# Kernel tuning notes

Measured on AMD Instinct MI355X. Metric: run time of the kernel, lower is better.

## Reference

```python
import jax, jax.numpy as jnp
import numpy as np

# dims
H = 2048      # hidden_size
NH = 16       # num q heads
NKV = 8       # num kv heads
D = 128       # head_dim
E = 16        # routed experts
K = 4         # top_k
I = 1024      # moe_intermediate_size (per routed expert)
SI = 1024     # shared expert intermediate (moe_intermediate * num_shared)
T = 2048      # tokens
EPS = 1e-5
THETA = 10000.0
RSF = 1.0     # router_scaling_factor


def setup_inputs() -> dict:
    key = jax.random.key(0)
    ks = jax.random.split(key, 10)
    s = 0.02
    return {
        "positions": jnp.arange(T, dtype=jnp.int32),
        "hidden_states": jax.random.normal(ks[0], (T, H), jnp.float32),
        "qkv_w": jax.random.normal(ks[1], (H, (NH + 2 * NKV) * D), jnp.float32) * s,
        "o_w": jax.random.normal(ks[2], (NH * D, H), jnp.float32) * s,
        "q_norm_w": jnp.ones((D,), jnp.float32),
        "k_norm_w": jnp.ones((D,), jnp.float32),
        "ln1_w": jnp.ones((H,), jnp.float32),
        "ln2_w": jnp.ones((H,), jnp.float32),
        "gate_w": jax.random.normal(ks[3], (H, E), jnp.float32) * s,
        "expert_bias": jax.random.normal(ks[4], (E,), jnp.float32) * 0.1,
        "shared_gu_w": jax.random.normal(ks[5], (H, 2 * SI), jnp.float32) * s,
        "shared_down_w": jax.random.normal(ks[6], (SI, H), jnp.float32) * s,
        "exp_gu_w": jax.random.normal(ks[7], (E, H, 2 * I), jnp.float32) * s,
        "exp_down_w": jax.random.normal(ks[8], (E, I, H), jnp.float32) * s,
    }


def _rmsnorm(x, w):
    v = jnp.mean(x * x, axis=-1, keepdims=True)
    return x * jax.lax.rsqrt(v + EPS) * w


def _rope(x, cos, sin):
    # neox style: rotate halves. x: [T, heads, D]; cos/sin: [T, 1, D//2]
    x1, x2 = x[..., : D // 2], x[..., D // 2 :]
    return jnp.concatenate([x1 * cos - x2 * sin, x2 * cos + x1 * sin], axis=-1)


def reference(positions, hidden_states, qkv_w, o_w, q_norm_w, k_norm_w,
              ln1_w, ln2_w, gate_w, expert_bias, shared_gu_w, shared_down_w,
              exp_gu_w, exp_down_w):
    hs = hidden_states
    # --- attention block ---
    x = _rmsnorm(hs, ln1_w)
    qkv = x @ qkv_w
    q = qkv[:, : NH * D].reshape(T, NH, D)
    k = qkv[:, NH * D : NH * D + NKV * D].reshape(T, NKV, D)
    v = qkv[:, NH * D + NKV * D :].reshape(T, NKV, D)
    # per-head qk RMSNorm
    q = _rmsnorm(q, q_norm_w)
    k = _rmsnorm(k, k_norm_w)
    # rotary embedding
    inv_freq = 1.0 / (THETA ** (jnp.arange(0, D, 2, dtype=jnp.float32) / D))
    ang = positions.astype(jnp.float32)[:, None] * inv_freq  # [T, D/2]
    cos = jnp.cos(ang)[:, None, :]
    sin = jnp.sin(ang)[:, None, :]
    q = _rope(q, cos, sin)
    k = _rope(k, cos, sin)
    # GQA: repeat kv heads
    rep = NH // NKV
    k = jnp.repeat(k, rep, axis=1)  # [T, NH, D]
    v = jnp.repeat(v, rep, axis=1)
    scores = jnp.einsum('qhd,khd->hqk', q, k) * (D ** -0.5)
    causal = jnp.tril(jnp.ones((T, T), dtype=bool))
    scores = jnp.where(causal[None], scores, -1e30)
    attn = jax.nn.softmax(scores, axis=-1)
    ao = jnp.einsum('hqk,khd->qhd', attn, v).reshape(T, NH * D)
    h = hs + ao @ o_w
    # --- MoE block ---
    x2 = _rmsnorm(h, ln2_w)
    router_logits = x2 @ gate_w  # fp32 gate
    sig = jax.nn.sigmoid(router_logits)
    biased = sig + expert_bias  # correction bias only used for selection
    _, top_idx = jax.lax.top_k(biased, K)  # [T, K]
    w = jnp.take_along_axis(sig, top_idx, axis=-1)
    w = w / jnp.sum(w, axis=-1, keepdims=True) * RSF  # renormalize + routed scaling
    combine = jnp.sum(jax.nn.one_hot(top_idx, E, dtype=x2.dtype) * w[..., None], axis=1)  # [T, E]
    # routed experts (dense-masked reference for the grouped GEMM)
    gu = jnp.einsum('th,ehi->eti', x2, exp_gu_w)  # [E, T, 2I]
    act = jax.nn.silu(gu[..., :I]) * gu[..., I:]
    routed = jnp.einsum('eti,eih->eth', act, exp_down_w)
    routed = jnp.einsum('eth,te->th', routed, combine)
    # shared expert
    sgu = x2 @ shared_gu_w
    shared = (jax.nn.silu(sgu[:, :SI]) * sgu[:, SI:]) @ shared_down_w
    return h + routed + shared
```

## Files before the change

kernel.cpp:

```cpp
#include <hip/hip_runtime.h>
#include <math.h>

#define T_ 2048
#define H_ 2048
#define NH_ 16
#define NKV_ 8
#define D_ 128
#define E_ 16
#define I_ 1024
#define SI_ 1024

typedef _Float16 half8 __attribute__((ext_vector_type(8)));
typedef _Float16 half4_t __attribute__((ext_vector_type(4)));
typedef float f32x4 __attribute__((ext_vector_type(4)));

#define MFMA32(a,b,c) __builtin_amdgcn_mfma_f32_16x16x32_f16((a),(b),(c),0,0,0)

__device__ __constant__ float LO_S = 2048.0f;
__device__ __constant__ float LO_I = 1.0f/2048.0f;
#define EPS_ 1e-5f

#define GL16(gp, lp) __builtin_amdgcn_global_load_lds( \
    (const __attribute__((address_space(1))) unsigned int*)(const void*)(gp), \
    (__attribute__((address_space(3))) unsigned int*)(void*)(lp), 16, 0, 0)

__global__ void tables_k(const int* __restrict__ pos, float* __restrict__ cosT, float* __restrict__ sinT) {
  int t = blockIdx.x;
  int j = threadIdx.x;
  float pf = (float)pow(10000.0, (double)j / 64.0);
  float invf = 1.0f / pf;
  float ang = (float)pos[t] * invf;
  cosT[t*64 + j] = (float)cos((double)ang);
  sinT[t*64 + j] = (float)sin((double)ang);
}

__global__ __launch_bounds__(256) void rmsnorm_k(const float* __restrict__ x, const float* __restrict__ w,
                                                 _Float16* __restrict__ oh, _Float16* __restrict__ ol) {
  int row = blockIdx.x;
  const float* xr = x + (size_t)row * H_;
  int tid = threadIdx.x;
  float4 a = *(const float4*)(xr + tid*8);
  float4 b = *(const float4*)(xr + tid*8 + 4);
  float ss = a.x*a.x + a.y*a.y + a.z*a.z + a.w*a.w + b.x*b.x + b.y*b.y + b.z*b.z + b.w*b.w;
  #pragma unroll
  for (int m = 1; m < 64; m <<= 1) ss += __shfl_xor(ss, m);
  __shared__ float wsum[4];
  int wid = tid >> 6, lane = tid & 63;
  if (lane == 0) wsum[wid] = ss;
  __syncthreads();
  float tot = wsum[0] + wsum[1] + wsum[2] + wsum[3];
  float rinv = 1.0f / sqrtf(tot / (float)H_ + EPS_);
  const float* av = (const float*)&a;
  const float* bv = (const float*)&b;
  #pragma unroll
  for (int j = 0; j < 8; ++j) {
    float xv = (j < 4) ? av[j] : bv[j-4];
    float val = xv * rinv * w[tid*8 + j];
    _Float16 h = (_Float16)val;
    size_t o = (size_t)row*H_ + tid*8 + j;
    oh[o] = h;
    ol[o] = (_Float16)((val - (float)h) * LO_S);
  }
}

__global__ __launch_bounds__(128) void qkvpost_k(
    const float* __restrict__ qkv, const float* __restrict__ qnw, const float* __restrict__ knw,
    const float* __restrict__ cosT, const float* __restrict__ sinT,
    _Float16* __restrict__ qh, _Float16* __restrict__ ql,
    _Float16* __restrict__ kh, _Float16* __restrict__ kl,
    _Float16* __restrict__ vth, _Float16* __restrict__ vtl) {
  int t = blockIdx.x, u = blockIdx.y, d = threadIdx.x;
  float val = qkv[(size_t)t*4096 + u*128 + d];
  __shared__ float sv[128];
  __shared__ float ssum[2];
  if (u < 24) {
    float ss = val * val;
    #pragma unroll
    for (int m = 1; m < 64; m <<= 1) ss += __shfl_xor(ss, m);
    if ((d & 63) == 0) ssum[d >> 6] = ss;
    __syncthreads();
    float rinv = 1.0f / sqrtf((ssum[0] + ssum[1]) / 128.0f + EPS_);
    const float* nw = (u < 16) ? qnw : knw;
    float nv = val * rinv * nw[d];
    sv[d] = nv;
    __syncthreads();
    int j = d & 63;
    float c = cosT[t*64 + j], s = sinT[t*64 + j];
    float x1 = sv[j], x2 = sv[j + 64];
    float o = (d < 64) ? (x1*c - x2*s) : (x2*c + x1*s);
    _Float16 hv = (_Float16)o;
    _Float16 lv = (_Float16)((o - (float)hv) * LO_S);
    if (u < 16) { size_t off = ((size_t)u*T_ + t)*D_ + d; qh[off] = hv; ql[off] = lv; }
    else { size_t off = ((size_t)(u-16)*T_ + t)*D_ + d; kh[off] = hv; kl[off] = lv; }
  } else {
    int kv = u - 24;
    _Float16 hv = (_Float16)val;
    _Float16 lv = (_Float16)((val - (float)hv) * LO_S);
    size_t off = ((size_t)kv*D_ + d)*T_ + t;
    vth[off] = hv; vtl[off] = lv;
  }
}

template<bool SPL>
__global__ __launch_bounds__(256) void transpose_k(const float* __restrict__ in, _Float16* __restrict__ oh,
                                                   _Float16* __restrict__ ol, int R, int C) {
  size_t zo = (size_t)blockIdx.z * R * C;
  in += zo; oh += zo; if (SPL) ol += zo;
  __shared__ float tile[64][68];
  const int c0 = blockIdx.x*64, r0 = blockIdx.y*64;
  const int tid = threadIdx.x;
  const int lr = tid >> 4;
  const int lc = (tid & 15) * 4;
  #pragma unroll
  for (int rg = 0; rg < 4; ++rg) {
    float4 v = *(const float4*)(in + (size_t)(r0 + rg*16 + lr)*C + c0 + lc);
    *(float4*)&tile[rg*16 + lr][lc] = v;
  }
  __syncthreads();
  const int orow = tid >> 2;
  const int oc   = (tid & 3) * 16;
  half8 h0v, h1v, l0v, l1v;
  #pragma unroll
  for (int j = 0; j < 16; ++j) {
    float f = tile[oc + j][orow];
    _Float16 h = (_Float16)f;
    if (j < 8) { h0v[j] = h; if (SPL) l0v[j] = (_Float16)((f - (float)h) * LO_S); }
    else       { h1v[j-8] = h; if (SPL) l1v[j-8] = (_Float16)((f - (float)h) * LO_S); }
  }
  const size_t ob = (size_t)(c0 + orow)*R + r0 + oc;
  *(half8*)(oh + ob)     = h0v;
  *(half8*)(oh + ob + 8) = h1v;
  if (SPL) { *(half8*)(ol + ob) = l0v; *(half8*)(ol + ob + 8) = l1v; }
}

__global__ __launch_bounds__(256) void transpose_gu_k(const float* __restrict__ in, _Float16* __restrict__ out,
                                                      int R, int Ih) {
  size_t zi = (size_t)blockIdx.z * R * 2 * Ih;
  in += zi; out += zi;
  __shared__ float tg[64][36], tu[64][36];
  const int j0 = blockIdx.x*32, h0 = blockIdx.y*64;
  const int tid = threadIdx.x;
  const int lh = tid >> 2;
  const int lj = (tid & 3) * 8;
  const int C = 2*Ih;
  const float* src = in + (size_t)(h0 + lh)*C + j0 + lj;
  float4 ga = *(const float4*)(src);
  float4 gb = *(const float4*)(src + 4);
  float4 ua = *(const float4*)(src + Ih);
  float4 ub = *(const float4*)(src + Ih + 4);
  *(float4*)&tg[lh][lj]   = ga;
  *(float4*)&tg[lh][lj+4] = gb;
  *(float4*)&tu[lh][lj]   = ua;
  *(float4*)&tu[lh][lj+4] = ub;
  __syncthreads();
  const int oj = tid >> 3;
  const int p  = (tid >> 2) & 1;
  const int oc = (tid & 3) * 16;
  float (*sel)[36] = p ? tu : tg;
  half8 a, b;
  #pragma unroll
  for (int j = 0; j < 16; ++j) {
    float f = sel[oc + j][oj];
    if (j < 8) a[j] = (_Float16)f; else b[j-8] = (_Float16)f;
  }
  const size_t ob = (size_t)(2*(j0 + oj) + p)*R + h0 + oc;
  *(half8*)(out + ob)     = a;
  *(half8*)(out + ob + 8) = b;
}

__global__ __launch_bounds__(256) void attn_k(
    const _Float16* __restrict__ qh_, const _Float16* __restrict__ ql_,
    const _Float16* __restrict__ kh_, const _Float16* __restrict__ kl_,
    const _Float16* __restrict__ vh_, const _Float16* __restrict__ vl_,
    _Float16* __restrict__ aoh, _Float16* __restrict__ aol) {
  __shared__ _Float16 sK [2][4096];
  __shared__ _Float16 sKl[2][4096];
  __shared__ _Float16 sV [2][4096];
  __shared__ _Float16 sVl[2][4096];
  const int head = blockIdx.x;
  const int y = blockIdx.y;
  const int tile = (y < 16) ? (31 - 2*y) : (2*(y-16));
  const int kvh = head >> 1;
  const int wid = threadIdx.x >> 6, lane = threadIdx.x & 63;
  const int fr = lane & 15, fs = lane >> 4;
  const float scale = 0.08838834764831845f;

  const char* kbC  = (const char*)(kh_ + (size_t)kvh*T_*D_);
  const char* kbCl = (const char*)(kl_ + (size_t)kvh*T_*D_);
  const char* vbC  = (const char*)(vh_ + (size_t)kvh*D_*T_);
  const char* vbCl = (const char*)(vl_ + (size_t)kvh*D_*T_);

  auto stage = [&](int buf, int kvt) {
    #pragma unroll
    for (int i = 0; i < 2; ++i) {
      const int off  = wid*2048 + i*1024;
      const int loff = off + lane*16;
      const int r  = loff >> 8;
      const int u  = (loff >> 4) & 15;
      const int us = u ^ (r & 7);
      const size_t gb = ((size_t)(kvt + r) << 8) + ((size_t)us << 4);
      GL16(kbC  + gb, (char*)&sK [buf][0] + off);
      GL16(kbCl + gb, (char*)&sKl[buf][0] + off);
      const int d   = loff >> 6;
      const int uv  = (loff >> 4) & 3;
      const int uvs = uv ^ ((d >> 2) & 3);
      const size_t gvb = (size_t)d*(T_*2) + (size_t)kvt*2 + ((size_t)uvs << 4);
      GL16(vbC  + gvb, (char*)&sV [buf][0] + off);
      GL16(vbCl + gvb, (char*)&sVl[buf][0] + off);
    }
  };

  const int q0 = tile*64 + wid*16;
  const int qrow = q0 + fr;
  const _Float16* qb_  = qh_ + ((size_t)head*T_ + qrow)*D_;
  const _Float16* qlb_ = ql_ + ((size_t)head*T_ + qrow)*D_;
  half8 qf[4], qfl[4];
  #pragma unroll
  for (int s = 0; s < 4; ++s) {
    qf[s]  = *(const half8*)(qb_  + s*32 + fs*8);
    qfl[s] = *(const half8*)(qlb_ + s*32 + fs*8);
  }
  float m = -1e30f, lsum = 0.f;
  f32x4 oacc[8] = {};
  f32x4 oacc2[8] = {};
  const int nc = 2*tile + 2;

  stage(0, 0);
  #pragma unroll 1
  for (int c = 0; c < nc; ++c) {
    const int kvt = c*32;
    const int buf = c & 1;
    __syncthreads();
    if (c + 1 < nc) stage(buf ^ 1, kvt + 32);

    f32x4 sa = {0,0,0,0}, sa2 = {0,0,0,0}, sb = {0,0,0,0}, sb2 = {0,0,0,0};
    __builtin_amdgcn_s_setprio(1);
    #pragma unroll
    for (int s = 0; s < 4; ++s) {
      const int rA = fr, rB = fr + 16;
      const int eA = (((4*s + fs) ^ (rA & 7)) << 3);
      const int eB = (((4*s + fs) ^ (rB & 7)) << 3);
      half8 kfA  = *(const half8*)&sK [buf][rA*128 + eA];
      half8 kflA = *(const half8*)&sKl[buf][rA*128 + eA];
      half8 kfB  = *(const half8*)&sK [buf][rB*128 + eB];
      half8 kflB = *(const half8*)&sKl[buf][rB*128 + eB];
      sa  = MFMA32(kfA, qf[s], sa);
      sa2 = MFMA32(kfA, qfl[s], sa2);
      sa2 = MFMA32(kflA, qf[s], sa2);
      sb  = MFMA32(kfB, qf[s], sb);
      sb2 = MFMA32(kfB, qfl[s], sb2);
      sb2 = MFMA32(kflB, qf[s], sb2);
    }
    __builtin_amdgcn_s_setprio(0);

    float sv[8];
    #pragma unroll
    for (int r = 0; r < 4; ++r) {
      float xA = (sa[r] + sa2[r]*LO_I) * scale;
      sv[r] = (kvt + fs*4 + r > qrow) ? -INFINITY : xA;
      float xB = (sb[r] + sb2[r]*LO_I) * scale;
      sv[4+r] = (kvt + 16 + fs*4 + r > qrow) ? -INFINITY : xB;
    }
    float tm = -INFINITY;
    #pragma unroll
    for (int j = 0; j < 8; ++j) tm = fmaxf(tm, sv[j]);
    tm = fmaxf(tm, __shfl_xor(tm, 16));
    tm = fmaxf(tm, __shfl_xor(tm, 32));
    if (tm > m + 8.f) {
      float f = __expf(m - tm);
      lsum *= f;
      #pragma unroll
      for (int db = 0; db < 8; ++db) { oacc[db] *= f; oacc2[db] *= f; }
      m = tm;
    }
    float p[8]; float ps = 0.f;
    #pragma unroll
    for (int j = 0; j < 8; ++j) { p[j] = __expf(sv[j] - m); ps += p[j]; }
    ps += __shfl_xor(ps, 16);
    ps += __shfl_xor(ps, 32);
    lsum += ps;
    half8 ph, pl;
    #pragma unroll
    for (int j = 0; j < 8; ++j) {
      _Float16 hp = (_Float16)p[j];
      ph[j] = hp;
      pl[j] = (_Float16)((p[j] - (float)hp) * LO_S);
    }

    __builtin_amdgcn_s_setprio(1);
    #pragma unroll
    for (int db = 0; db < 8; ++db) {
      const int d0 = db*16 + fr;
      const int base = d0*32;
      const int sw = (d0 >> 2) & 3;
      const int e1 = ((((fs>>1)    ) ^ sw) << 3) + (fs & 1)*4;
      const int e2 = (((2 + (fs>>1)) ^ sw) << 3) + (fs & 1)*4;
      half4_t v0  = *(const half4_t*)&sV [buf][base + e1];
      half4_t v1  = *(const half4_t*)&sV [buf][base + e2];
      half4_t v0l = *(const half4_t*)&sVl[buf][base + e1];
      half4_t v1l = *(const half4_t*)&sVl[buf][base + e2];
      half8 vf, vfl;
      #pragma unroll
      for (int j = 0; j < 4; ++j) { vf[j] = v0[j]; vf[4+j] = v1[j]; vfl[j] = v0l[j]; vfl[4+j] = v1l[j]; }
      oacc[db]  = MFMA32(vf, ph, oacc[db]);
      oacc2[db] = MFMA32(vf, pl, oacc2[db]);
      oacc2[db] = MFMA32(vfl, ph, oacc2[db]);
    }
    __builtin_amdgcn_s_setprio(0);
  }

  float inv = 1.0f / lsum;
  #pragma unroll
  for (int db = 0; db < 8; ++db) {
    #pragma unroll
    for (int r = 0; r < 4; ++r) {
      float val = (oacc[db][r] + oacc2[db][r]*LO_I) * inv;
      int dd = db*16 + fs*4 + r;
      size_t off = (size_t)qrow*(NH_*D_) + head*D_ + dd;
      _Float16 hv = (_Float16)val;
      aoh[off] = hv;
      aol[off] = (_Float16)((val - (float)hv) * LO_S);
    }
  }
}

__global__ __launch_bounds__(256) void router_k(const _Float16* __restrict__ x2h, const _Float16* __restrict__ x2l,
    const float* __restrict__ gw, const float* __restrict__ eb,
    int* __restrict__ cnt, int* __restrict__ list, float* __restrict__ wl) {
  int t = blockIdx.x*4 + (threadIdx.x >> 6);
  int lane = threadIdx.x & 63;
  const _Float16* xh = x2h + (size_t)t*H_;
  const _Float16* xl = x2l + (size_t)t*H_;
  f32x4 a0 = {0,0,0,0}, a1 = {0,0,0,0}, a2 = {0,0,0,0}, a3 = {0,0,0,0};
  for (int h = lane; h < H_; h += 64) {
    float xv = (float)xh[h] + (float)xl[h] * LO_I;
    const float* g = gw + (size_t)h*16;
    a0 += xv * (*(const f32x4*)(g));
    a1 += xv * (*(const f32x4*)(g+4));
    a2 += xv * (*(const f32x4*)(g+8));
    a3 += xv * (*(const f32x4*)(g+12));
  }
  float acc[16];
  #pragma unroll
  for (int j = 0; j < 4; ++j) { acc[j]=a0[j]; acc[4+j]=a1[j]; acc[8+j]=a2[j]; acc[12+j]=a3[j]; }
  #pragma unroll
  for (int mm = 1; mm < 64; mm <<= 1) {
    #pragma unroll
    for (int e2 = 0; e2 < 16; ++e2) acc[e2] += __shfl_xor(acc[e2], mm);
  }
  if (lane == 0) {
    float sig[16], biased[16];
    #pragma unroll
    for (int e2 = 0; e2 < 16; ++e2) {
      float s = 1.0f / (1.0f + expf(-acc[e2]));
      sig[e2] = s; biased[e2] = s + eb[e2];
    }
    int sel[4]; float wv[4]; float wsum = 0.f;
    unsigned used = 0;
    for (int j = 0; j < 4; ++j) {
      int bi = -1; float bv = -1e30f;
      for (int e2 = 0; e2 < 16; ++e2)
        if (!((used >> e2) & 1) && biased[e2] > bv) { bv = biased[e2]; bi = e2; }
      used |= 1u << bi;
      sel[j] = bi; wv[j] = sig[bi]; wsum += sig[bi];
    }
    for (int j = 0; j < 4; ++j) {
      int e2 = sel[j];
      int pos = atomicAdd(&cnt[e2], 1);
      list[e2*T_ + pos] = t;
      wl[e2*T_ + pos] = wv[j] / wsum;
    }
  }
}

__global__ void scan_k(const int* __restrict__ cnt, int* __restrict__ base) {
  if (threadIdx.x == 0 && blockIdx.x == 0) {
    int s = 0;
    for (int e2 = 0; e2 < 16; ++e2) { base[e2] = s; s += cnt[e2]; }
  }
}

struct GArgs {
  const _Float16* Ah; const _Float16* Al;
  const _Float16* Bh; const _Float16* Bl;
  int M, N, K;
  const int* rowlist; const float* wlist; const int* cnt; const int* base;
  float* C; const float* res; _Float16* act; float* outAt; int ldc;
};

template<int MODE, bool SPLIT, int DEPTH>
__global__ __launch_bounds__(512, 4) void gemm_k(GArgs p) {
  constexpr int LPS = SPLIT ? 4 : 2;
  const int e = blockIdx.z;
  const int M = p.cnt ? p.cnt[e] : p.M;
  const int m0 = blockIdx.y * 128;
  if (m0 >= M) return;
  const int n0 = blockIdx.x * 128;
  const int tid = threadIdx.x;
  const int wid = tid >> 6, lane = tid & 63;

  __shared__ _Float16 sA[DEPTH][4096];
  __shared__ _Float16 sB[DEPTH][4096];
  __shared__ _Float16 sAl[SPLIT ? DEPTH : 1][SPLIT ? 4096 : 8];
  __shared__ _Float16 sBl[SPLIT ? DEPTH : 1][SPLIT ? 4096 : 8];

  const int srow = tid >> 2;
  const int slot = ((tid & 3) ^ (srow & 3)) * 16;
  const int ldsOff = wid * 1024;
  size_t aIdx;
  if constexpr (MODE == 2) {
    if (p.rowlist) {
      int tok = p.rowlist[(size_t)e * T_ + m0 + srow];
      tok = tok < 0 ? 0 : (tok > T_ - 1 ? T_ - 1 : tok);
      aIdx = (size_t)tok;
    } else aIdx = (size_t)(m0 + srow);
  } else if constexpr (MODE == 3) {
    aIdx = (size_t)p.base[e] + m0 + srow;
  } else {
    aIdx = (size_t)(m0 + srow);
  }
  const char* aPtr  = (const char*)(p.Ah + aIdx * (size_t)p.K) + slot;
  const char* alPtr = SPLIT ? (const char*)(p.Al + aIdx * (size_t)p.K) + slot : aPtr;
  const size_t bIdx = (size_t)e * p.N + n0 + srow;
  const char* bPtr  = (const char*)(p.Bh + bIdx * (size_t)p.K) + slot;
  const char* blPtr = SPLIT ? (const char*)(p.Bl + bIdx * (size_t)p.K) + slot : bPtr;

  auto stage = [&](int buf, int kb) {
    GL16(aPtr + kb, (char*)&sA[buf][0] + ldsOff);
    GL16(bPtr + kb, (char*)&sB[buf][0] + ldsOff);
    if constexpr (SPLIT) {
      GL16(alPtr + kb, (char*)&sAl[buf][0] + ldsOff);
      GL16(blPtr + kb, (char*)&sBl[buf][0] + ldsOff);
    }
  };

  const int wr = (wid >> 2) * 64, wc = (wid & 3) * 32;
  const int fr = lane & 15, fs = lane >> 4;

  f32x4 acc[4][2] = {};
  f32x4 acc2[4][2] = {};

  const int nt = p.K >> 5;
  stage(0, 0);
  if constexpr (DEPTH == 3) { if (nt > 1) stage(1, 64); }

  for (int t = 0; t < nt; ++t) {
    if constexpr (DEPTH == 3) {
      if (t + 2 < nt) stage((t + 2) % 3, (t + 2) * 64);
      __builtin_amdgcn_sched_barrier(0);
      if (t + 2 < nt)      asm volatile("s_waitcnt vmcnt(%0)" :: "i"(2*LPS) : "memory");
      else if (t + 1 < nt) asm volatile("s_waitcnt vmcnt(%0)" :: "i"(LPS)   : "memory");
      else                 asm volatile("s_waitcnt vmcnt(0)" ::: "memory");
    } else {
      if (t + 1 < nt) {
        stage((t + 1) & 1, (t + 1) * 64);
        __builtin_amdgcn_sched_barrier(0);
        asm volatile("s_waitcnt vmcnt(%0)" :: "i"(LPS) : "memory");
      } else {
        __builtin_amdgcn_sched_barrier(0);
        asm volatile("s_waitcnt vmcnt(0)" ::: "memory");
      }
    }
    __builtin_amdgcn_s_barrier();
    __builtin_amdgcn_sched_barrier(0);

    const int cb = (DEPTH == 3) ? (t % 3) : (t & 1);
    half8 ah[4], bh[2], al[4], bl[2];
    #pragma unroll
    for (int i = 0; i < 4; ++i) {
      const int pa = (fs ^ ((wr + i*16 + fr) & 3)) * 8;
      ah[i] = *(const half8*)&sA[cb][(wr + i*16 + fr)*32 + pa];
      if constexpr (SPLIT) al[i] = *(const half8*)&sAl[cb][(wr + i*16 + fr)*32 + pa];
    }
    #pragma unroll
    for (int i = 0; i < 2; ++i) {
      const int pb = (fs ^ ((wc + i*16 + fr) & 3)) * 8;
      bh[i] = *(const half8*)&sB[cb][(wc + i*16 + fr)*32 + pb];
      if constexpr (SPLIT) bl[i] = *(const half8*)&sBl[cb][(wc + i*16 + fr)*32 + pb];
    }
    __builtin_amdgcn_s_setprio(1);
    #pragma unroll
    for (int mi = 0; mi < 4; ++mi) {
      #pragma unroll
      for (int ni = 0; ni < 2; ++ni) {
        acc[mi][ni] = MFMA32(ah[mi], bh[ni], acc[mi][ni]);
        if constexpr (SPLIT) {
          acc2[mi][ni] = MFMA32(ah[mi], bl[ni], acc2[mi][ni]);
          acc2[mi][ni] = MFMA32(al[mi], bh[ni], acc2[mi][ni]);
        }
      }
    }
    __builtin_amdgcn_s_setprio(0);
    __builtin_amdgcn_sched_barrier(0);
    __builtin_amdgcn_s_barrier();
    __builtin_amdgcn_sched_barrier(0);
  }

  const int actld = p.N >> 1;
  #pragma unroll
  for (int mi = 0; mi < 4; ++mi) {
    #pragma unroll
    for (int ni = 0; ni < 2; ++ni) {
      f32x4 v4 = acc[mi][ni];
      if constexpr (SPLIT) v4 = v4 + acc2[mi][ni] * LO_I;
      const int colb = n0 + wc + ni*16 + fr;
      #pragma unroll
      for (int r = 0; r < 4; ++r) {
        const int row = m0 + wr + mi*16 + fs*4 + r;
        float val = v4[r];
        if constexpr (MODE == 0) {
          if (row < M) p.C[(size_t)row * p.ldc + colb] = val;
        } else if constexpr (MODE == 1) {
          if (row < M) p.C[(size_t)row * p.ldc + colb] = p.res[(size_t)row * p.ldc + colb] + val;
        } else if constexpr (MODE == 2) {
          float other = __shfl_xor(val, 1);
          float g = (fr & 1) ? other : val;
          float u = (fr & 1) ? val : other;
          float a = g / (1.0f + __expf(-g)) * u;
          if (!(fr & 1) && row < M) {
            size_t ar = (size_t)(p.base ? p.base[e] : 0) + row;
            p.act[ar * (size_t)actld + (colb >> 1)] = (_Float16)a;
          }
        } else {
          if (row < M) {
            int tok = p.rowlist[(size_t)e * T_ + row];
            float w = p.wlist[(size_t)e * T_ + row];
            atomicAdd(&p.outAt[(size_t)tok * p.ldc + colb], val * w);
          }
        }
      }
    }
  }
}

extern "C" void kernel_launch(void* const* d_in, const int* in_sizes, int n_in,
                              void* d_out, int out_size, void* d_ws, size_t ws_size,
                              hipStream_t stream) {
  (void)in_sizes; (void)n_in; (void)out_size; (void)ws_size;
  const int*   positions = (const int*)  d_in[0];
  const float* hidden    = (const float*)d_in[1];
  const float* qkv_w     = (const float*)d_in[2];
  const float* o_w       = (const float*)d_in[3];
  const float* q_norm_w  = (const float*)d_in[4];
  const float* k_norm_w  = (const float*)d_in[5];
  const float* ln1_w     = (const float*)d_in[6];
  const float* ln2_w     = (const float*)d_in[7];
  const float* gate_w    = (const float*)d_in[8];
  const float* ebias     = (const float*)d_in[9];
  const float* sgu_w     = (const float*)d_in[10];
  const float* sdown_w   = (const float*)d_in[11];
  const float* egu_w     = (const float*)d_in[12];
  const float* edown_w   = (const float*)d_in[13];
  float* out = (float*)d_out;

  char* wsp = (char*)d_ws;
  size_t off = 0;
  auto alloc = [&](size_t bytes) -> void* {
    void* p = wsp + off;
    off = (off + bytes + 255) & ~(size_t)255;
    return p;
  };
  float*    cosT   = (float*)   alloc((size_t)T_*64*4);
  float*    sinT   = (float*)   alloc((size_t)T_*64*4);
  _Float16* x_h    = (_Float16*)alloc((size_t)T_*H_*2);
  _Float16* x_l    = (_Float16*)alloc((size_t)T_*H_*2);
  float*    qkvb   = (float*)   alloc((size_t)T_*4096*4);
  _Float16* q_h    = (_Float16*)alloc((size_t)NH_*T_*D_*2);
  _Float16* q_l    = (_Float16*)alloc((size_t)NH_*T_*D_*2);
  _Float16* k_h    = (_Float16*)alloc((size_t)NKV_*T_*D_*2);
  _Float16* k_l    = (_Float16*)alloc((size_t)NKV_*T_*D_*2);
  _Float16* vt_h   = (_Float16*)alloc((size_t)NKV_*T_*D_*2);
  _Float16* vt_l   = (_Float16*)alloc((size_t)NKV_*T_*D_*2);
  _Float16* ao_h   = (_Float16*)alloc((size_t)T_*NH_*D_*2);
  _Float16* ao_l   = (_Float16*)alloc((size_t)T_*NH_*D_*2);
  float*    hbuf   = (float*)   alloc((size_t)T_*H_*4);
  _Float16* x2_h   = (_Float16*)alloc((size_t)T_*H_*2);
  _Float16* x2_l   = (_Float16*)alloc((size_t)T_*H_*2);
  _Float16* qkvwT_h= (_Float16*)alloc((size_t)4096*H_*2);
  _Float16* qkvwT_l= (_Float16*)alloc((size_t)4096*H_*2);
  _Float16* owT_h  = (_Float16*)alloc((size_t)H_*H_*2);
  _Float16* owT_l  = (_Float16*)alloc((size_t)H_*H_*2);
  _Float16* sguT   = (_Float16*)alloc((size_t)2*SI_*H_*2);
  _Float16* sdownT = (_Float16*)alloc((size_t)H_*SI_*2);
  _Float16* eguT   = (_Float16*)alloc((size_t)E_*2*I_*H_*2);
  _Float16* edownT = (_Float16*)alloc((size_t)E_*H_*I_*2);
  _Float16* act_s  = (_Float16*)alloc((size_t)T_*SI_*2);
  _Float16* act_e  = (_Float16*)alloc((size_t)(T_*4 + 512)*I_*2);
  int*   cnt   = (int*)  alloc(E_*4);
  int*   ebase = (int*)  alloc(E_*4);
  int*   list  = (int*)  alloc((size_t)E_*T_*4);
  float* wlst  = (float*)alloc((size_t)E_*T_*4);

  hipMemsetAsync(cnt, 0, E_*4, stream);
  tables_k<<<T_, 64, 0, stream>>>(positions, cosT, sinT);

  transpose_k<true ><<<dim3(4096/64, H_/64, 1), 256, 0, stream>>>(qkv_w, qkvwT_h, qkvwT_l, H_, 4096);
  transpose_k<true ><<<dim3(H_/64,  H_/64, 1), 256, 0, stream>>>(o_w, owT_h, owT_l, H_, H_);
  transpose_gu_k    <<<dim3(SI_/32, H_/64, 1), 256, 0, stream>>>(sgu_w, sguT, H_, SI_);
  transpose_k<false><<<dim3(H_/64, SI_/64, 1), 256, 0, stream>>>(sdown_w, sdownT, nullptr, SI_, H_);
  transpose_gu_k    <<<dim3(I_/32,  H_/64, E_), 256, 0, stream>>>(egu_w, eguT, H_, I_);
  transpose_k<false><<<dim3(H_/64,  I_/64, E_), 256, 0, stream>>>(edown_w, edownT, nullptr, I_, H_);

  rmsnorm_k<<<T_, 256, 0, stream>>>(hidden, ln1_w, x_h, x_l);

  { GArgs g{}; g.Ah=x_h; g.Al=x_l; g.Bh=qkvwT_h; g.Bl=qkvwT_l; g.M=T_; g.N=4096; g.K=H_;
    g.C=qkvb; g.ldc=4096;
    gemm_k<0,true,2><<<dim3(4096/128, T_/128, 1), 512, 0, stream>>>(g); }

  qkvpost_k<<<dim3(T_, 32, 1), 128, 0, stream>>>(qkvb, q_norm_w, k_norm_w, cosT, sinT,
                                                 q_h, q_l, k_h, k_l, vt_h, vt_l);

  attn_k<<<dim3(NH_, 32), 256, 0, stream>>>(q_h, q_l, k_h, k_l, vt_h, vt_l, ao_h, ao_l);

  { GArgs g{}; g.Ah=ao_h; g.Al=ao_l; g.Bh=owT_h; g.Bl=owT_l; g.M=T_; g.N=H_; g.K=H_;
    g.C=hbuf; g.res=hidden; g.ldc=H_;
    gemm_k<1,true,2><<<dim3(H_/128, T_/128, 1), 512, 0, stream>>>(g); }

  rmsnorm_k<<<T_, 256, 0, stream>>>(hbuf, ln2_w, x2_h, x2_l);

  router_k<<<T_/4, 256, 0, stream>>>(x2_h, x2_l, gate_w, ebias, cnt, list, wlst);
  scan_k<<<1, 64, 0, stream>>>(cnt, ebase);

  { GArgs g{}; g.Ah=x2_h; g.Bh=sguT; g.M=T_; g.N=2*SI_; g.K=H_; g.act=act_s;
    gemm_k<2,false,3><<<dim3(2*SI_/128, T_/128, 1), 512, 0, stream>>>(g); }

  { GArgs g{}; g.Ah=act_s; g.Bh=sdownT; g.M=T_; g.N=H_; g.K=SI_;
    g.C=out; g.res=hbuf; g.ldc=H_;
    gemm_k<1,false,3><<<dim3(H_/128, T_/128, 1), 512, 0, stream>>>(g); }

  { GArgs g{}; g.Ah=x2_h; g.Bh=eguT; g.M=T_; g.N=2*I_; g.K=H_;
    g.rowlist=list; g.cnt=cnt; g.base=ebase; g.act=act_e;
    gemm_k<2,false,3><<<dim3(2*I_/128, T_/128, E_), 512, 0, stream>>>(g); }

  { GArgs g{}; g.Ah=act_e; g.Bh=edownT; g.M=T_; g.N=H_; g.K=I_;
    g.rowlist=list; g.wlist=wlst; g.cnt=cnt; g.base=ebase;
    g.outAt=out; g.ldc=H_;
    gemm_k<3,false,3><<<dim3(H_/128, T_/128, E_), 512, 0, stream>>>(g); }
}
```

Before: 994.9 us.

## Replace atomic expert scatter with staged output and gather-combine kernel; restructure qkvpost

The routed down-projection no longer does float atomicAdd into the output per token. It now writes weighted rows contiguously into a staging buffer that reuses the qkv scratch, and a new combine kernel gathers the four expert rows per token through a token-to-slot map recorded by the router. This removes atomic contention and makes the summation order deterministic, at the cost of an extra pass over T*4*H floats. The qkv post-processing kernel is also reworked so one block handles a whole token, with each wave doing one head and the norm reduced by wave shuffles without LDS or barriers.

```diff
diff --git a/kernel.cpp b/kernel.cpp
--- a/kernel.cpp
+++ b/kernel.cpp
@@ -63,41 +63,54 @@
   }
 }
 
-__global__ __launch_bounds__(128) void qkvpost_k(
+__global__ __launch_bounds__(256) void qkvpost_k(
     const float* __restrict__ qkv, const float* __restrict__ qnw, const float* __restrict__ knw,
     const float* __restrict__ cosT, const float* __restrict__ sinT,
     _Float16* __restrict__ qh, _Float16* __restrict__ ql,
     _Float16* __restrict__ kh, _Float16* __restrict__ kl,
     _Float16* __restrict__ vth, _Float16* __restrict__ vtl) {
-  int t = blockIdx.x, u = blockIdx.y, d = threadIdx.x;
-  float val = qkv[(size_t)t*4096 + u*128 + d];
-  __shared__ float sv[128];
-  __shared__ float ssum[2];
-  if (u < 24) {
-    float ss = val * val;
-    #pragma unroll
-    for (int m = 1; m < 64; m <<= 1) ss += __shfl_xor(ss, m);
-    if ((d & 63) == 0) ssum[d >> 6] = ss;
-    __syncthreads();
-    float rinv = 1.0f / sqrtf((ssum[0] + ssum[1]) / 128.0f + EPS_);
-    const float* nw = (u < 16) ? qnw : knw;
-    float nv = val * rinv * nw[d];
-    sv[d] = nv;
-    __syncthreads();
-    int j = d & 63;
-    float c = cosT[t*64 + j], s = sinT[t*64 + j];
-    float x1 = sv[j], x2 = sv[j + 64];
-    float o = (d < 64) ? (x1*c - x2*s) : (x2*c + x1*s);
-    _Float16 hv = (_Float16)o;
-    _Float16 lv = (_Float16)((o - (float)hv) * LO_S);
-    if (u < 16) { size_t off = ((size_t)u*T_ + t)*D_ + d; qh[off] = hv; ql[off] = lv; }
-    else { size_t off = ((size_t)(u-16)*T_ + t)*D_ + d; kh[off] = hv; kl[off] = lv; }
-  } else {
-    int kv = u - 24;
-    _Float16 hv = (_Float16)val;
-    _Float16 lv = (_Float16)((val - (float)hv) * LO_S);
-    size_t off = ((size_t)kv*D_ + d)*T_ + t;
-    vth[off] = hv; vtl[off] = lv;
+  const int t = blockIdx.x;
+  const int wid = threadIdx.x >> 6, lane = threadIdx.x & 63;
+  const float* src = qkv + (size_t)t*4096;
+  const float c = cosT[t*64 + lane];
+  const float s = sinT[t*64 + lane];
+  #pragma unroll
+  for (int it = 0; it < 8; ++it) {
+    const int u = it*4 + wid;
+    float x1 = src[u*128 + lane];
+    float x2 = src[u*128 + 64 + lane];
+    if (u < 24) {
+      float ss = x1*x1 + x2*x2;
+      #pragma unroll
+      for (int m = 1; m < 64; m <<= 1) ss += __shfl_xor(ss, m);
+      float rinv = 1.0f / sqrtf(ss / 128.0f + EPS_);
+      const float* nw = (u < 16) ? qnw : knw;
+      float n1 = x1 * rinv * nw[lane];
+      float n2 = x2 * rinv * nw[lane + 64];
+      float o1 = n1*c - n2*s;
+      float o2 = n2*c + n1*s;
+      _Float16 h1 = (_Float16)o1, h2 = (_Float16)o2;
+      _Float16 l1 = (_Float16)((o1 - (float)h1) * LO_S);
+      _Float16 l2 = (_Float16)((o2 - (float)h2) * LO_S);
+      if (u < 16) {
+        size_t off = ((size_t)u*T_ + t)*D_;
+        qh[off + lane] = h1; qh[off + 64 + lane] = h2;
+        ql[off + lane] = l1; ql[off + 64 + lane] = l2;
+      } else {
+        size_t off = ((size_t)(u-16)*T_ + t)*D_;
+        kh[off + lane] = h1; kh[off + 64 + lane] = h2;
+        kl[off + lane] = l1; kl[off + 64 + lane] = l2;
+      }
+    } else {
+      const int kv = u - 24;
+      _Float16 h1 = (_Float16)x1, h2 = (_Float16)x2;
+      _Float16 l1 = (_Float16)((x1 - (float)h1) * LO_S);
+      _Float16 l2 = (_Float16)((x2 - (float)h2) * LO_S);
+      size_t o1 = ((size_t)kv*D_ + lane)*T_ + t;
+      size_t o2 = ((size_t)kv*D_ + 64 + lane)*T_ + t;
+      vth[o1] = h1; vth[o2] = h2;
+      vtl[o1] = l1; vtl[o2] = l2;
+    }
   }
 }
 
@@ -326,7 +339,7 @@
 
 __global__ __launch_bounds__(256) void router_k(const _Float16* __restrict__ x2h, const _Float16* __restrict__ x2l,
     const float* __restrict__ gw, const float* __restrict__ eb,
-    int* __restrict__ cnt, int* __restrict__ list, float* __restrict__ wl) {
+    int* __restrict__ cnt, int* __restrict__ list, float* __restrict__ wl, int* __restrict__ tokslot) {
   int t = blockIdx.x*4 + (threadIdx.x >> 6);
   int lane = threadIdx.x & 63;
   const _Float16* xh = x2h + (size_t)t*H_;
@@ -369,6 +382,7 @@
       int pos = atomicAdd(&cnt[e2], 1);
       list[e2*T_ + pos] = t;
       wl[e2*T_ + pos] = wv[j] / wsum;
+      tokslot[t*4 + j] = e2*T_ + pos;
     }
   }
 }
@@ -378,6 +392,29 @@
     int s = 0;
     for (int e2 = 0; e2 < 16; ++e2) { base[e2] = s; s += cnt[e2]; }
   }
+}
+
+__global__ __launch_bounds__(256) void combine_k(const int* __restrict__ tokslot, const int* __restrict__ base,
+                                                 const float* __restrict__ eout, float* __restrict__ outp) {
+  const int t = blockIdx.x, tid = threadIdx.x;
+  const int col = tid * 8;
+  int r[4];
+  #pragma unroll
+  for (int j = 0; j < 4; ++j) {
+    int s = tokslot[t*4 + j];
+    r[j] = base[s >> 11] + (s & 2047);
+  }
+  float* op = outp + (size_t)t*H_ + col;
+  f32x4 a0 = *(const f32x4*)(op);
+  f32x4 a1 = *(const f32x4*)(op + 4);
+  #pragma unroll
+  for (int j = 0; j < 4; ++j) {
+    const float* er = eout + (size_t)r[j]*H_ + col;
+    a0 += *(const f32x4*)(er);
+    a1 += *(const f32x4*)(er + 4);
+  }
+  *(f32x4*)(op)     = a0;
+  *(f32x4*)(op + 4) = a1;
 }
 
 struct GArgs {
@@ -523,9 +560,8 @@
           }
         } else {
           if (row < M) {
-            int tok = p.rowlist[(size_t)e * T_ + row];
             float w = p.wlist[(size_t)e * T_ + row];
-            atomicAdd(&p.outAt[(size_t)tok * p.ldc + colb], val * w);
+            p.outAt[((size_t)p.base[e] + row) * p.ldc + colb] = val * w;
           }
         }
       }
@@ -586,10 +622,12 @@
   _Float16* edownT = (_Float16*)alloc((size_t)E_*H_*I_*2);
   _Float16* act_s  = (_Float16*)alloc((size_t)T_*SI_*2);
   _Float16* act_e  = (_Float16*)alloc((size_t)(T_*4 + 512)*I_*2);
-  int*   cnt   = (int*)  alloc(E_*4);
-  int*   ebase = (int*)  alloc(E_*4);
-  int*   list  = (int*)  alloc((size_t)E_*T_*4);
-  float* wlst  = (float*)alloc((size_t)E_*T_*4);
+  int*   cnt     = (int*)  alloc(E_*4);
+  int*   ebase   = (int*)  alloc(E_*4);
+  int*   list    = (int*)  alloc((size_t)E_*T_*4);
+  float* wlst    = (float*)alloc((size_t)E_*T_*4);
+  int*   tokslot = (int*)  alloc((size_t)T_*4*4);
+  float* eout = qkvb;
 
   hipMemsetAsync(cnt, 0, E_*4, stream);
   tables_k<<<T_, 64, 0, stream>>>(positions, cosT, sinT);
@@ -607,8 +645,8 @@
     g.C=qkvb; g.ldc=4096;
     gemm_k<0,true,2><<<dim3(4096/128, T_/128, 1), 512, 0, stream>>>(g); }
 
-  qkvpost_k<<<dim3(T_, 32, 1), 128, 0, stream>>>(qkvb, q_norm_w, k_norm_w, cosT, sinT,
-                                                 q_h, q_l, k_h, k_l, vt_h, vt_l);
+  qkvpost_k<<<T_, 256, 0, stream>>>(qkvb, q_norm_w, k_norm_w, cosT, sinT,
+                                    q_h, q_l, k_h, k_l, vt_h, vt_l);
 
   attn_k<<<dim3(NH_, 32), 256, 0, stream>>>(q_h, q_l, k_h, k_l, vt_h, vt_l, ao_h, ao_l);
 
@@ -618,7 +656,7 @@
 
   rmsnorm_k<<<T_, 256, 0, stream>>>(hbuf, ln2_w, x2_h, x2_l);
 
-  router_k<<<T_/4, 256, 0, stream>>>(x2_h, x2_l, gate_w, ebias, cnt, list, wlst);
+  router_k<<<T_/4, 256, 0, stream>>>(x2_h, x2_l, gate_w, ebias, cnt, list, wlst, tokslot);
   scan_k<<<1, 64, 0, stream>>>(cnt, ebase);
 
   { GArgs g{}; g.Ah=x2_h; g.Bh=sguT; g.M=T_; g.N=2*SI_; g.K=H_; g.act=act_s;
@@ -633,7 +671,9 @@
     gemm_k<2,false,3><<<dim3(2*I_/128, T_/128, E_), 512, 0, stream>>>(g); }
 
   { GArgs g{}; g.Ah=act_e; g.Bh=edownT; g.M=T_; g.N=H_; g.K=I_;
-    g.rowlist=list; g.wlist=wlst; g.cnt=cnt; g.base=ebase;
-    g.outAt=out; g.ldc=H_;
+    g.wlist=wlst; g.cnt=cnt; g.base=ebase;
+    g.outAt=eout; g.ldc=H_;
     gemm_k<3,false,3><<<dim3(H_/128, T_/128, E_), 512, 0, stream>>>(g); }
-}
+
+  combine_k<<<T_, 256, 0, stream>>>(tokslot, ebase, eout, out);
+}
```

Result: no change. 978.5 us (-1.6%).
